# Kernel tuning notes

Hardware: AMD Instinct MI355X
Metric: run time of the kernel (lower is better)

## Reference

```python
import jax, jax.numpy as jnp
import numpy as np

HEADS = 30
HEAD_DIM = 64
DIM = HEADS * HEAD_DIM  # 1920
TXT = 226
VID = 2048
EPS = 1e-5


def setup_inputs() -> dict:
    key = jax.random.key(0)
    ks = jax.random.split(key, 12)
    s = 1.0 / np.sqrt(DIM)
    return {
        "hidden_states": jax.random.normal(ks[0], (1, VID, DIM), jnp.float32),
        "encoder_hidden_states": jax.random.normal(ks[1], (1, TXT, DIM), jnp.float32),
        "rope_cos": jax.random.uniform(ks[2], (VID, HEAD_DIM), jnp.float32, -1.0, 1.0),
        "rope_sin": jax.random.uniform(ks[3], (VID, HEAD_DIM), jnp.float32, -1.0, 1.0),
        "Wq": jax.random.normal(ks[4], (DIM, DIM), jnp.float32) * s,
        "bq": jnp.zeros((DIM,), jnp.float32),
        "Wk": jax.random.normal(ks[5], (DIM, DIM), jnp.float32) * s,
        "bk": jnp.zeros((DIM,), jnp.float32),
        "Wv": jax.random.normal(ks[6], (DIM, DIM), jnp.float32) * s,
        "bv": jnp.zeros((DIM,), jnp.float32),
        "ln_q_w": jnp.ones((HEAD_DIM,), jnp.float32),
        "ln_q_b": jnp.zeros((HEAD_DIM,), jnp.float32),
        "ln_k_w": jnp.ones((HEAD_DIM,), jnp.float32),
        "ln_k_b": jnp.zeros((HEAD_DIM,), jnp.float32),
        "Wo": jax.random.normal(ks[7], (DIM, DIM), jnp.float32) * s,
        "bo": jnp.zeros((DIM,), jnp.float32),
    }


def _layernorm(x, w, b):
    mu = jnp.mean(x, axis=-1, keepdims=True)
    var = jnp.var(x, axis=-1, keepdims=True)
    return (x - mu) * jax.lax.rsqrt(var + EPS) * w + b


def _apply_rope(x, cos, sin):
    # x: [B,H,S_vid,D]; cos/sin: [S_vid,D]. Interleaved-pair rotation (diffusers use_real, unbind_dim=-1).
    xr = x[..., 0::2]
    xi = x[..., 1::2]
    rot = jnp.stack([-xi, xr], axis=-1).reshape(x.shape)
    return x * cos + rot * sin


def reference(hidden_states, encoder_hidden_states, rope_cos, rope_sin,
              Wq, bq, Wk, bk, Wv, bv, ln_q_w, ln_q_b, ln_k_w, ln_k_b, Wo, bo):
    T = encoder_hidden_states.shape[1]
    h = jnp.concatenate([encoder_hidden_states, hidden_states], axis=1)  # [B,S,D]
    B, S, _ = h.shape

    def proj(W, bias):
        y = h @ W.T + bias
        return y.reshape(B, S, HEADS, HEAD_DIM).transpose(0, 2, 1, 3)  # [B,H,S,d]

    q = proj(Wq, bq)
    k = proj(Wk, bk)
    v = proj(Wv, bv)

    q = _layernorm(q, ln_q_w, ln_q_b)
    k = _layernorm(k, ln_k_w, ln_k_b)

    # rotary embedding applied only to the image/video tokens
    q = jnp.concatenate([q[:, :, :T], _apply_rope(q[:, :, T:], rope_cos, rope_sin)], axis=2)
    k = jnp.concatenate([k[:, :, :T], _apply_rope(k[:, :, T:], rope_cos, rope_sin)], axis=2)

    scale = 1.0 / np.sqrt(HEAD_DIM)
    scores = jnp.einsum("bhqd,bhkd->bhqk", q, k) * scale
    attn = jax.nn.softmax(scores, axis=-1)
    out = jnp.einsum("bhqk,bhkd->bhqd", attn, v)

    out = out.transpose(0, 2, 1, 3).reshape(B, S, DIM)
    out = out @ Wo.T + bo
    return out[:, T:], out[:, :T]
```

## Files before the change

### kernel.cpp

```cpp
#include <hip/hip_runtime.h>
#include <hip/hip_bf16.h>

typedef __hip_bfloat16 bf16;
using f32x4 = __attribute__((ext_vector_type(4))) float;
using f32x16 = __attribute__((ext_vector_type(16))) float;
using s16x8 = __attribute__((ext_vector_type(8))) short;

#define S_TOT 2274
#define S_PAD 2304
#define TTXT 226
#define DIMN 1920
#define NH 30
#define HD 64
#define NQKV 5760
#define QSCALE 0.1803368801f
#define NSPLIT 4
#define SMAX 20.0f

#define GLOAD_LDS16(g, l)                                                              \
  __builtin_amdgcn_global_load_lds((const __attribute__((address_space(1))) void*)(g), \
                                   (__attribute__((address_space(3))) void*)(l), 16, 0, 0)

__device__ __forceinline__ int xcd_swz(int orig, int nwg) {
  const int q = nwg >> 3, r = nwg & 7;
  const int xcd = orig & 7, pos = orig >> 3;
  return (xcd < r ? xcd * (q + 1) : r * (q + 1) + (xcd - r) * q) + pos;
}

__global__ void k_prep_all(const float* __restrict__ hid, const float* __restrict__ enc,
                           const float* __restrict__ Wq, const float* __restrict__ Wk,
                           const float* __restrict__ Wv, const float* __restrict__ Wo,
                           bf16* __restrict__ h_bf, bf16* __restrict__ wqkv,
                           bf16* __restrict__ wo_bf) {
  const long T1 = (long)S_PAD * DIMN;
  const long PER = (long)DIMN * DIMN;
  long i4 = ((long)blockIdx.x * blockDim.x + threadIdx.x) * 4;
  if (i4 >= T1 + 4 * PER) return;
  float4 v = make_float4(0.f, 0.f, 0.f, 0.f);
  bf16* dst;
  long di;
  if (i4 < T1) {
    int s = (int)(i4 / DIMN);
    if (s < TTXT)
      v = *reinterpret_cast<const float4*>(enc + i4);
    else if (s < S_TOT)
      v = *reinterpret_cast<const float4*>(hid + i4 - (long)TTXT * DIMN);
    dst = h_bf;
    di = i4;
  } else if (i4 < T1 + 3 * PER) {
    const long j = i4 - T1;
    const float* src = (j < PER) ? (Wq + j) : (j < 2 * PER) ? (Wk + j - PER) : (Wv + j - 2 * PER);
    v = *reinterpret_cast<const float4*>(src);
    dst = wqkv;
    di = j;
  } else {
    const long j = i4 - T1 - 3 * PER;
    v = *reinterpret_cast<const float4*>(Wo + j);
    dst = wo_bf;
    di = j;
  }
  union {
    bf16 b[4];
    short4 s4;
  } o;
  o.b[0] = __float2bfloat16(v.x);
  o.b[1] = __float2bfloat16(v.y);
  o.b[2] = __float2bfloat16(v.z);
  o.b[3] = __float2bfloat16(v.w);
  *reinterpret_cast<short4*>(dst + di) = o.s4;
}

#define NKT32 60
#define QBUF 24576
__global__ __launch_bounds__(512, 4) void k_gemm_qkv11(
    const bf16* __restrict__ A, const bf16* __restrict__ B, const float* __restrict__ bq,
    const float* __restrict__ bk, const float* __restrict__ bv, const float* __restrict__ lqw,
    const float* __restrict__ lqb, const float* __restrict__ lkw, const float* __restrict__ lkb,
    const float* __restrict__ cosT, const float* __restrict__ sinT, bf16* __restrict__ qb,
    bf16* __restrict__ kbf, bf16* __restrict__ vt) {
  __shared__ __align__(16) char smem[3 * QBUF];
  const int tid = threadIdx.x;
  const int w = tid >> 6, lane = tid & 63;
  const int clo = lane & 15, lhi = lane >> 4;
  const int wr = w >> 1, wc = w & 1;
  const int swz = xcd_swz(blockIdx.y * 45 + blockIdx.x, 405);
  const int m0 = (swz / 45) * 256, n0 = (swz % 45) * 128;

  const int u1 = 512 + tid;
  const long ga0 = (long)(m0 + (tid >> 2)) * DIMN + (((tid & 3) ^ ((tid >> 3) & 3)) * 8);
  const long ga1 = (long)(m0 + (u1 >> 2)) * DIMN + (((u1 & 3) ^ ((u1 >> 3) & 3)) * 8);
  const long gb0 = (long)(n0 + (tid >> 2)) * DIMN + (((tid & 3) ^ ((tid >> 3) & 3)) * 8);
  const int wbase = w * 1024;

  auto stage = [&](int b, int kt) {
    char* Ab = &smem[b * QBUF];
    char* Bb = Ab + 16384;
    const int ko = kt * 32;
    GLOAD_LDS16(A + ga0 + ko, Ab + wbase);
    GLOAD_LDS16(A + ga1 + ko, Ab + 8192 + wbase);
    GLOAD_LDS16(B + gb0 + ko, Bb + wbase);
  };

  auto rdf = [&](const char* base, int row) {
    return *reinterpret_cast<const s16x8*>(base + row * 64 + ((lhi ^ ((row >> 1) & 3)) * 16));
  };

  f32x4 acc[4][4] = {};

  stage(0, 0);
  stage(1, 1);
  for (int t = 0; t < NKT32; ++t) {
    if (t < NKT32 - 1)
      asm volatile("s_waitcnt vmcnt(3)" ::: "memory");
    else
      asm volatile("s_waitcnt vmcnt(0)" ::: "memory");
    __builtin_amdgcn_s_barrier();
    if (t + 2 < NKT32) stage((t + 2) % 3, t + 2);
    const char* Ab = &smem[(t % 3) * QBUF];
    const char* Bb = Ab + 16384;
    s16x8 af[4], bfr[4];
#pragma unroll
    for (int m = 0; m < 4; ++m) af[m] = rdf(Ab, wr * 64 + m * 16 + clo);
#pragma unroll
    for (int n = 0; n < 4; ++n) bfr[n] = rdf(Bb, wc * 64 + n * 16 + clo);
    __builtin_amdgcn_s_setprio(1);
#pragma unroll
    for (int m = 0; m < 4; ++m)
#pragma unroll
      for (int n = 0; n < 4; ++n)
        acc[m][n] = __builtin_amdgcn_mfma_f32_16x16x32_bf16(af[m], bfr[n], acc[m][n], 0, 0, 0);
    __builtin_amdgcn_s_setprio(0);
  }
  __syncthreads();

  const int gcol0 = n0 + wc * 64;
  const int sect = gcol0 / DIMN;
  const int hcol = gcol0 - sect * DIMN;
  const int head = hcol >> 6;
  const int row0 = m0 + wr * 64;

  if (sect < 2) {
    const float* bias = sect ? bk : bq;
    const float* lw = sect ? lkw : lqw;
    const float* lb = sect ? lkb : lqb;
    bf16* dst = sect ? kbf : qb;
    const float oscale = sect ? 1.f : QSCALE;
    float bb[4], lww[4], lbb[4];
#pragma unroll
    for (int n = 0; n < 4; ++n) {
      const int d = (n << 4) + clo;
      bb[n] = bias[hcol + d];
      lww[n] = lw[d];
      lbb[n] = lb[d];
    }
#pragma unroll
    for (int m = 0; m < 4; ++m) {
#pragma unroll
      for (int r = 0; r < 4; ++r) {
        const int row = row0 + m * 16 + lhi * 4 + r;
        float x[4];
#pragma unroll
        for (int n = 0; n < 4; ++n) x[n] = acc[m][n][r] + bb[n];
        float s_ = (x[0] + x[1]) + (x[2] + x[3]);
        float q_ = x[0] * x[0];
        q_ = fmaf(x[1], x[1], q_);
        q_ = fmaf(x[2], x[2], q_);
        q_ = fmaf(x[3], x[3], q_);
#pragma unroll
        for (int off = 1; off <= 8; off <<= 1) {
          s_ += __shfl_xor(s_, off);
          q_ += __shfl_xor(q_, off);
        }
        const float mu = s_ * (1.f / 64.f);
        const float var = q_ * (1.f / 64.f) - mu * mu;
        const float rst = rsqrtf(var + 1e-5f);
        float xn[4];
#pragma unroll
        for (int n = 0; n < 4; ++n) xn[n] = (x[n] - mu) * rst * lww[n] + lbb[n];
        const bool dorope = (row >= TTXT) && (row < S_TOT);
        if (dorope) {
          const float* cr = cosT + (long)(row - TTXT) * HD;
          const float* sr2 = sinT + (long)(row - TTXT) * HD;
#pragma unroll
          for (int n = 0; n < 4; ++n) {
            const int d = (n << 4) + clo;
            const float p = __shfl_xor(xn[n], 1);
            xn[n] = xn[n] * cr[d] + ((clo & 1) ? p : -p) * sr2[d];
          }
        }
#pragma unroll
        for (int n = 0; n < 4; ++n)
          dst[((long)head * S_PAD + row) * HD + (n << 4) + clo] =
              __float2bfloat16(xn[n] * oscale);
      }
    }
  } else {
    float bb[4];
#pragma unroll
    for (int n = 0; n < 4; ++n) bb[n] = bv[hcol + (n << 4) + clo];
    bf16* Lp = reinterpret_cast<bf16*>(smem + w * 9216);
#pragma unroll
    for (int m = 0; m < 4; ++m)
#pragma unroll
      for (int n = 0; n < 4; ++n)
#pragma unroll
        for (int r = 0; r < 4; ++r)
          Lp[((n << 4) + clo) * 72 + m * 16 + lhi * 4 + r] =
              __float2bfloat16(acc[m][n][r] + bb[n]);
    const int dsub = lane >> 3, sc = lane & 7;
#pragma unroll
    for (int it = 0; it < 8; ++it) {
      const int d = it * 8 + dsub;
      s16x8 v = *reinterpret_cast<const s16x8*>(&Lp[d * 72 + sc * 8]);
      *reinterpret_cast<s16x8*>(vt + ((long)head * HD + d) * S_PAD + row0 + sc * 8) = v;
    }
  }
}

__global__ __launch_bounds__(256, 4) void k_gemm_proj11(const bf16* __restrict__ A,
                                                        const bf16* __restrict__ B,
                                                        float* __restrict__ C,
                                                        const float* __restrict__ bias) {
  __shared__ __align__(16) char smem[3 * 12288];
  const int tid = threadIdx.x;
  const int w = tid >> 6, lane = tid & 63;
  const int clo = lane & 15, lhi = lane >> 4;
  const int wr = w >> 1, wc = w & 1;
  const int swz = xcd_swz(blockIdx.y * 30 + blockIdx.x, 540);
  const int m0 = (swz / 30) * 128, n0 = (swz % 30) * 64;

  const int u1 = 256 + tid;
  const long ga0 = (long)(m0 + (tid >> 2)) * DIMN + (((tid & 3) ^ ((tid >> 3) & 3)) * 8);
  const long ga1 = (long)(m0 + (u1 >> 2)) * DIMN + (((u1 & 3) ^ ((u1 >> 3) & 3)) * 8);
  const long gb0 = (long)(n0 + (tid >> 2)) * DIMN + (((tid & 3) ^ ((tid >> 3) & 3)) * 8);
  const int wbase = w * 1024;

  auto stage = [&](int b, int kt) {
    char* Ab = &smem[b * 12288];
    char* Bb = Ab + 8192;
    const int ko = kt * 32;
    GLOAD_LDS16(A + ga0 + ko, Ab + wbase);
    GLOAD_LDS16(A + ga1 + ko, Ab + 4096 + wbase);
    GLOAD_LDS16(B + gb0 + ko, Bb + wbase);
  };

  auto rdf = [&](const char* base, int row) {
    return *reinterpret_cast<const s16x8*>(base + row * 64 + ((lhi ^ ((row >> 1) & 3)) * 16));
  };

  f32x4 acc[4][2] = {};

  stage(0, 0);
  stage(1, 1);
  for (int t = 0; t < NKT32; ++t) {
    if (t < NKT32 - 1)
      asm volatile("s_waitcnt vmcnt(3)" ::: "memory");
    else
      asm volatile("s_waitcnt vmcnt(0)" ::: "memory");
    __builtin_amdgcn_s_barrier();
    if (t + 2 < NKT32) stage((t + 2) % 3, t + 2);
    const char* Ab = &smem[(t % 3) * 12288];
    const char* Bb = Ab + 8192;
    s16x8 af[4], bfr[2];
#pragma unroll
    for (int m = 0; m < 4; ++m) af[m] = rdf(Ab, wr * 64 + m * 16 + clo);
#pragma unroll
    for (int n = 0; n < 2; ++n) bfr[n] = rdf(Bb, wc * 32 + n * 16 + clo);
    __builtin_amdgcn_s_setprio(1);
#pragma unroll
    for (int m = 0; m < 4; ++m)
#pragma unroll
      for (int n = 0; n < 2; ++n)
        acc[m][n] = __builtin_amdgcn_mfma_f32_16x16x32_bf16(af[m], bfr[n], acc[m][n], 0, 0, 0);
    __builtin_amdgcn_s_setprio(0);
  }
#pragma unroll
  for (int n = 0; n < 2; ++n) {
    const int col = n0 + wc * 32 + n * 16 + clo;
    const float bvv = bias[col];
#pragma unroll
    for (int m = 0; m < 4; ++m) {
#pragma unroll
      for (int r = 0; r < 4; ++r) {
        const int row = m0 + wr * 64 + m * 16 + lhi * 4 + r;
        if (row < S_TOT) {
          const int dst = (row >= TTXT) ? (row - TTXT) : (row + (S_TOT - TTXT));
          C[(long)dst * DIMN + col] = acc[m][n][r] + bvv;
        }
      }
    }
  }
}

__global__ __launch_bounds__(512, 4) void k_flash14(const bf16* __restrict__ qb,
                                                    const bf16* __restrict__ kbf,
                                                    const bf16* __restrict__ vt,
                                                    bf16* __restrict__ po,
                                                    float* __restrict__ pl) {
  __shared__ __align__(16) char smem[32768];
  const int h = blockIdx.x, qt = blockIdx.y, ks = blockIdx.z;
  const int tid = threadIdx.x, w = tid >> 6, lane = tid & 63;
  const int l31 = lane & 31, hf = lane >> 5;
  const bf16* Qh = qb + (long)h * S_PAD * HD;
  const bf16* Kh = kbf + (long)h * S_PAD * HD;
  const bf16* Vh = vt + (long)h * HD * S_PAD;
  const int q0w = qt * 256 + w * 32;
  const int T0 = ks * 9;

  s16x8 qf[4];
#pragma unroll
  for (int t = 0; t < 4; ++t)
    qf[t] = *reinterpret_cast<const s16x8*>(Qh + (long)(q0w + l31) * HD + t * 16 + hf * 8);

  f32x16 accO[2] = {};
  f32x16 lacc = {};

  const s16x8 ones8 = {0x3F80, 0x3F80, 0x3F80, 0x3F80, 0x3F80, 0x3F80, 0x3F80, 0x3F80};

  const int sr = tid >> 3, sc8 = tid & 7;
  const long kg0 = (long)sr * HD + ((sc8 ^ (sr & 7)) * 8);
  const long vg0 = (long)sr * S_PAD + ((sc8 ^ (sr & 7)) * 8);
  const int ldsb = w * 1024;

  auto stage = [&](int b, int kb0) {
    char* Kb = &smem[b * 16384];
    char* Vb = &smem[b * 16384 + 8192];
    GLOAD_LDS16(Kh + (long)kb0 * HD + kg0, Kb + ldsb);
    GLOAD_LDS16(Vh + kb0 + vg0, Vb + ldsb);
  };

  auto ldsrd = [&](const char* base, int row, int c) {
    return *reinterpret_cast<const s16x8*>(base + row * 128 + ((c ^ (row & 7)) * 16));
  };
  auto pk2 = [&](float a, float b) -> unsigned {
    __hip_bfloat162 t = __float22bfloat162_rn(make_float2(a, b));
    return *reinterpret_cast<unsigned*>(&t);
  };

  stage(0, T0 * 64);
  __syncthreads();
  int cur = 0;
  for (int kt = 0; kt < 9; ++kt) {
    const int kb0 = (T0 + kt) * 64;
    if (kt + 1 < 9) stage(cur ^ 1, kb0 + 64);
    const char* Kb = &smem[cur * 16384];
    const char* Vb = &smem[cur * 16384 + 8192];

    f32x16 s0 = {}, s1 = {};
#pragma unroll
    for (int t = 0; t < 4; ++t) {
      s16x8 k0 = ldsrd(Kb, l31, 2 * t + hf);
      s16x8 k1 = ldsrd(Kb, 32 + l31, 2 * t + hf);
      s0 = __builtin_amdgcn_mfma_f32_32x32x16_bf16(k0, qf[t], s0, 0, 0, 0);
      s1 = __builtin_amdgcn_mfma_f32_32x32x16_bf16(k1, qf[t], s1, 0, 0, 0);
    }
    if (kb0 + 64 > S_TOT) {
#pragma unroll
      for (int j = 0; j < 16; ++j) {
        const int key = kb0 + (j & 3) + 8 * (j >> 2) + 4 * hf;
        if (key >= S_TOT) s0[j] = -1e30f;
        if (key + 32 >= S_TOT) s1[j] = -1e30f;
      }
    }
#pragma unroll
    for (int j = 0; j < 16; ++j) {
      s0[j] = exp2f(s0[j] - SMAX);
      s1[j] = exp2f(s1[j] - SMAX);
    }
    unsigned gw0[8], gw1[8];
#pragma unroll
    for (int i = 0; i < 4; ++i) {
      gw0[2 * i] = pk2(s0[4 * i], s0[4 * i + 1]);
      gw0[2 * i + 1] = pk2(s0[4 * i + 2], s0[4 * i + 3]);
      gw1[2 * i] = pk2(s1[4 * i], s1[4 * i + 1]);
      gw1[2 * i + 1] = pk2(s1[4 * i + 2], s1[4 * i + 3]);
    }
    s16x8 pa[4];
#pragma unroll
    for (int b = 0; b < 2; ++b) {
      unsigned* gw = b ? gw1 : gw0;
#pragma unroll
      for (int t = 0; t < 2; ++t) {
        auto rA = __builtin_amdgcn_permlane32_swap(gw[4 * t + 0], gw[4 * t + 2], false, false);
        auto rB = __builtin_amdgcn_permlane32_swap(gw[4 * t + 1], gw[4 * t + 3], false, false);
        union {
          unsigned u[4];
          s16x8 v;
        } A;
        A.u[0] = rA[0];
        A.u[1] = rB[0];
        A.u[2] = rA[1];
        A.u[3] = rB[1];
        pa[b * 2 + t] = A.v;
      }
    }
#pragma unroll
    for (int t4 = 0; t4 < 4; ++t4) {
      s16x8 v0 = ldsrd(Vb, l31, 2 * t4 + hf);
      s16x8 v1 = ldsrd(Vb, 32 + l31, 2 * t4 + hf);
      accO[0] = __builtin_amdgcn_mfma_f32_32x32x16_bf16(pa[t4], v0, accO[0], 0, 0, 0);
      accO[1] = __builtin_amdgcn_mfma_f32_32x32x16_bf16(pa[t4], v1, accO[1], 0, 0, 0);
      lacc = __builtin_amdgcn_mfma_f32_32x32x16_bf16(pa[t4], ones8, lacc, 0, 0, 0);
    }
    __syncthreads();
    cur ^= 1;
  }
  const long rowbase = ((long)(ks * NH + h)) * S_PAD + q0w;
  if (l31 == 0) {
#pragma unroll
    for (int j = 0; j < 16; ++j) pl[rowbase + (j & 3) + 8 * (j >> 2) + 4 * hf] = lacc[j];
  }
#pragma unroll
  for (int j = 0; j < 16; ++j) {
    const int pat = (j & 3) + 8 * (j >> 2) + 4 * hf;
    bf16* dst = po + (rowbase + pat) * HD + l31;
    dst[0] = __float2bfloat16(accO[0][j]);
    dst[32] = __float2bfloat16(accO[1][j]);
  }
}

__global__ __launch_bounds__(256) void k_combine4(const bf16* __restrict__ po,
                                                  const float* __restrict__ pl,
                                                  bf16* __restrict__ ao) {
  const int idx = blockIdx.x * 256 + threadIdx.x;
  const int d4 = (idx & 15) * 4;
  const int row = (idx >> 4) % S_PAD;
  const int h = idx / (S_PAD * 16);
  if (row >= S_TOT) return;
  float o[4] = {0.f, 0.f, 0.f, 0.f};
  float l = 0.f;
#pragma unroll
  for (int i = 0; i < NSPLIT; ++i) {
    const long r = ((long)(i * NH + h)) * S_PAD + row;
    const ushort4 p = *reinterpret_cast<const ushort4*>(po + r * HD + d4);
    o[0] += __uint_as_float((unsigned)p.x << 16);
    o[1] += __uint_as_float((unsigned)p.y << 16);
    o[2] += __uint_as_float((unsigned)p.z << 16);
    o[3] += __uint_as_float((unsigned)p.w << 16);
    l += pl[r];
  }
  const float inv = 1.f / l;
  union {
    bf16 b[4];
    short4 s4;
  } ob;
#pragma unroll
  for (int i = 0; i < 4; ++i) ob.b[i] = __float2bfloat16(o[i] * inv);
  *reinterpret_cast<short4*>(ao + (long)row * DIMN + h * HD + d4) = ob.s4;
}

extern "C" void kernel_launch(void* const* d_in, const int* in_sizes, int n_in, void* d_out,
                              int out_size, void* d_ws, size_t ws_size, hipStream_t stream) {
  const float* hid = (const float*)d_in[0];
  const float* enc = (const float*)d_in[1];
  const float* rc = (const float*)d_in[2];
  const float* rs = (const float*)d_in[3];
  const float* Wq = (const float*)d_in[4];
  const float* bq = (const float*)d_in[5];
  const float* Wk = (const float*)d_in[6];
  const float* bk = (const float*)d_in[7];
  const float* Wv = (const float*)d_in[8];
  const float* bv = (const float*)d_in[9];
  const float* lqw = (const float*)d_in[10];
  const float* lqb = (const float*)d_in[11];
  const float* lkw = (const float*)d_in[12];
  const float* lkb = (const float*)d_in[13];
  const float* Wo = (const float*)d_in[14];
  const float* bo = (const float*)d_in[15];
  float* out = (float*)d_out;

  char* ws = (char*)d_ws;
  size_t off = 0;
  bf16* po = (bf16*)(ws + off);
  off += (size_t)S_PAD * NQKV * 4;
  bf16* h_bf = (bf16*)(ws + off);
  off += (size_t)S_PAD * DIMN * 2;
  bf16* wqkv = (bf16*)(ws + off);
  off += (size_t)3 * DIMN * DIMN * 2;
  bf16* wo = (bf16*)(ws + off);
  off += (size_t)DIMN * DIMN * 2;
  bf16* q_bf = (bf16*)(ws + off);
  off += (size_t)NH * S_PAD * HD * 2;
  bf16* k_bf = (bf16*)(ws + off);
  off += (size_t)NH * S_PAD * HD * 2;
  bf16* vt_bf = (bf16*)(ws + off);
  off += (size_t)NH * HD * S_PAD * 2;
  bf16* at_bf = (bf16*)(ws + off);
  off += (size_t)S_PAD * DIMN * 2;

  float* pl = (float*)h_bf;

  const long PREP_N = ((long)S_PAD * DIMN + 4L * DIMN * DIMN) / 4;
  k_prep_all<<<(int)((PREP_N + 255) / 256), 256, 0, stream>>>(hid, enc, Wq, Wk, Wv, Wo, h_bf,
                                                              wqkv, wo);
  k_gemm_qkv11<<<dim3(45, 9), 512, 0, stream>>>(h_bf, wqkv, bq, bk, bv, lqw, lqb, lkw, lkb, rc,
                                                rs, q_bf, k_bf, vt_bf);
  k_flash14<<<dim3(NH, S_PAD / 256, NSPLIT), 512, 0, stream>>>(q_bf, k_bf, vt_bf, po, pl);
  k_combine4<<<NH * S_PAD * 16 / 256, 256, 0, stream>>>(po, pl, at_bf);
  k_gemm_proj11<<<dim3(30, 18), 256, 0, stream>>>(at_bf, wo, out, bo);
}
```

Before: 213.3 us.

## Deepen QKV GEMM K-tile to 64 and interleave loads with MFMA quadrants

```diff
diff --git a/kernel.cpp b/kernel.cpp
--- a/kernel.cpp
+++ b/kernel.cpp
@@ -70,15 +70,16 @@
   *reinterpret_cast<short4*>(dst + di) = o.s4;
 }
 
-#define NKT32 60
-#define QBUF 24576
-__global__ __launch_bounds__(512, 4) void k_gemm_qkv11(
+#define NKT64 30
+#define ABYTES 32768
+#define TBUF 49152
+__global__ __launch_bounds__(512, 1) void k_gemm_qkv12(
     const bf16* __restrict__ A, const bf16* __restrict__ B, const float* __restrict__ bq,
     const float* __restrict__ bk, const float* __restrict__ bv, const float* __restrict__ lqw,
     const float* __restrict__ lqb, const float* __restrict__ lkw, const float* __restrict__ lkb,
     const float* __restrict__ cosT, const float* __restrict__ sinT, bf16* __restrict__ qb,
     bf16* __restrict__ kbf, bf16* __restrict__ vt) {
-  __shared__ __align__(16) char smem[3 * QBUF];
+  __shared__ __align__(16) char smem[3 * TBUF];
   const int tid = threadIdx.x;
   const int w = tid >> 6, lane = tid & 63;
   const int clo = lane & 15, lhi = lane >> 4;
@@ -86,50 +87,135 @@
   const int swz = xcd_swz(blockIdx.y * 45 + blockIdx.x, 405);
   const int m0 = (swz / 45) * 256, n0 = (swz % 45) * 128;
 
-  const int u1 = 512 + tid;
-  const long ga0 = (long)(m0 + (tid >> 2)) * DIMN + (((tid & 3) ^ ((tid >> 3) & 3)) * 8);
-  const long ga1 = (long)(m0 + (u1 >> 2)) * DIMN + (((u1 & 3) ^ ((u1 >> 3) & 3)) * 8);
-  const long gb0 = (long)(n0 + (tid >> 2)) * DIMN + (((tid & 3) ^ ((tid >> 3) & 3)) * 8);
+  long ga[4], gb[2];
+#pragma unroll
+  for (int i = 0; i < 4; ++i) {
+    const int u = i * 512 + tid;
+    ga[i] = (long)(m0 + (u >> 3)) * DIMN + (((u & 7) ^ ((u >> 3) & 7)) * 8);
+  }
+#pragma unroll
+  for (int i = 0; i < 2; ++i) {
+    const int u = i * 512 + tid;
+    gb[i] = (long)(n0 + (u >> 3)) * DIMN + (((u & 7) ^ ((u >> 3) & 7)) * 8);
+  }
   const int wbase = w * 1024;
 
-  auto stage = [&](int b, int kt) {
-    char* Ab = &smem[b * QBUF];
-    char* Bb = Ab + 16384;
-    const int ko = kt * 32;
-    GLOAD_LDS16(A + ga0 + ko, Ab + wbase);
-    GLOAD_LDS16(A + ga1 + ko, Ab + 8192 + wbase);
-    GLOAD_LDS16(B + gb0 + ko, Bb + wbase);
-  };
-
-  auto rdf = [&](const char* base, int row) {
-    return *reinterpret_cast<const s16x8*>(base + row * 64 + ((lhi ^ ((row >> 1) & 3)) * 16));
+  auto stA = [&](int b, int kt, int i) {
+    GLOAD_LDS16(A + ga[i] + kt * 64, &smem[b * TBUF] + i * 8192 + wbase);
+  };
+  auto stB = [&](int b, int kt, int i) {
+    GLOAD_LDS16(B + gb[i] + kt * 64, &smem[b * TBUF] + ABYTES + i * 8192 + wbase);
+  };
+  auto stageAll = [&](int b, int kt) {
+#pragma unroll
+    for (int i = 0; i < 4; ++i) stA(b, kt, i);
+#pragma unroll
+    for (int i = 0; i < 2; ++i) stB(b, kt, i);
+  };
+
+  auto rdA = [&](const char* buf, int m, int k) {
+    const int row = wr * 64 + m * 16 + clo;
+    return *reinterpret_cast<const s16x8*>(buf + row * 128 + (((k * 4 + lhi) ^ (row & 7)) * 16));
+  };
+  auto rdB = [&](const char* buf, int n, int k) {
+    const int row = wc * 64 + n * 16 + clo;
+    return *reinterpret_cast<const s16x8*>(buf + ABYTES + row * 128 +
+                                           (((k * 4 + lhi) ^ (row & 7)) * 16));
   };
 
   f32x4 acc[4][4] = {};
-
-  stage(0, 0);
-  stage(1, 1);
-  for (int t = 0; t < NKT32; ++t) {
-    if (t < NKT32 - 1)
-      asm volatile("s_waitcnt vmcnt(3)" ::: "memory");
+  s16x8 a01[2][2], a23[2][2], b01[2][2], b23[2][2];
+
+  stageAll(0, 0);
+  stageAll(1, 1);
+  asm volatile("s_waitcnt vmcnt(6)" ::: "memory");
+  __builtin_amdgcn_s_barrier();
+
+  for (int t = 0; t < NKT64; ++t) {
+    const char* buf = &smem[(t % 3) * TBUF];
+    const bool pre = (t + 2 < NKT64);
+    const int nb = (t + 2) % 3;
+#pragma unroll
+    for (int m = 0; m < 2; ++m)
+#pragma unroll
+      for (int k = 0; k < 2; ++k) a01[m][k] = rdA(buf, m, k);
+#pragma unroll
+    for (int n = 0; n < 2; ++n)
+#pragma unroll
+      for (int k = 0; k < 2; ++k) b01[n][k] = rdB(buf, n, k);
+    if (pre) {
+      stA(nb, t + 2, 0);
+      stA(nb, t + 2, 1);
+    }
+    __builtin_amdgcn_s_barrier();
+    asm volatile("s_waitcnt lgkmcnt(0)" ::: "memory");
+    __builtin_amdgcn_s_setprio(1);
+#pragma unroll
+    for (int m = 0; m < 2; ++m)
+#pragma unroll
+      for (int n = 0; n < 2; ++n)
+#pragma unroll
+        for (int k = 0; k < 2; ++k)
+          acc[m][n] = __builtin_amdgcn_mfma_f32_16x16x32_bf16(a01[m][k], b01[n][k], acc[m][n], 0, 0, 0);
+    __builtin_amdgcn_s_setprio(0);
+    __builtin_amdgcn_s_barrier();
+#pragma unroll
+    for (int n = 0; n < 2; ++n)
+#pragma unroll
+      for (int k = 0; k < 2; ++k) b23[n][k] = rdB(buf, n + 2, k);
+    if (pre) {
+      stA(nb, t + 2, 2);
+      stA(nb, t + 2, 3);
+    }
+    __builtin_amdgcn_s_barrier();
+    asm volatile("s_waitcnt lgkmcnt(0)" ::: "memory");
+    __builtin_amdgcn_s_setprio(1);
+#pragma unroll
+    for (int m = 0; m < 2; ++m)
+#pragma unroll
+      for (int n = 0; n < 2; ++n)
+#pragma unroll
+        for (int k = 0; k < 2; ++k)
+          acc[m][n + 2] =
+              __builtin_amdgcn_mfma_f32_16x16x32_bf16(a01[m][k], b23[n][k], acc[m][n + 2], 0, 0, 0);
+    __builtin_amdgcn_s_setprio(0);
+    __builtin_amdgcn_s_barrier();
+#pragma unroll
+    for (int m = 0; m < 2; ++m)
+#pragma unroll
+      for (int k = 0; k < 2; ++k) a23[m][k] = rdA(buf, m + 2, k);
+    if (pre) {
+      stB(nb, t + 2, 0);
+      stB(nb, t + 2, 1);
+    }
+    __builtin_amdgcn_s_barrier();
+    asm volatile("s_waitcnt lgkmcnt(0)" ::: "memory");
+    __builtin_amdgcn_s_setprio(1);
+#pragma unroll
+    for (int m = 0; m < 2; ++m)
+#pragma unroll
+      for (int n = 0; n < 2; ++n)
+#pragma unroll
+        for (int k = 0; k < 2; ++k)
+          acc[m + 2][n] =
+              __builtin_amdgcn_mfma_f32_16x16x32_bf16(a23[m][k], b01[n][k], acc[m + 2][n], 0, 0, 0);
+    __builtin_amdgcn_s_setprio(0);
+    __builtin_amdgcn_s_barrier();
+    __builtin_amdgcn_s_setprio(1);
+#pragma unroll
+    for (int m = 0; m < 2; ++m)
+#pragma unroll
+      for (int n = 0; n < 2; ++n)
+#pragma unroll
+        for (int k = 0; k < 2; ++k)
+          acc[m + 2][n + 2] = __builtin_amdgcn_mfma_f32_16x16x32_bf16(a23[m][k], b23[n][k],
+                                                                     acc[m + 2][n + 2], 0, 0, 0);
+    __builtin_amdgcn_s_setprio(0);
+    if (pre)
+      asm volatile("s_waitcnt vmcnt(6)" ::: "memory");
     else
       asm volatile("s_waitcnt vmcnt(0)" ::: "memory");
     __builtin_amdgcn_s_barrier();
-    if (t + 2 < NKT32) stage((t + 2) % 3, t + 2);
-    const char* Ab = &smem[(t % 3) * QBUF];
-    const char* Bb = Ab + 16384;
-    s16x8 af[4], bfr[4];
-#pragma unroll
-    for (int m = 0; m < 4; ++m) af[m] = rdf(Ab, wr * 64 + m * 16 + clo);
-#pragma unroll
-    for (int n = 0; n < 4; ++n) bfr[n] = rdf(Bb, wc * 64 + n * 16 + clo);
-    __builtin_amdgcn_s_setprio(1);
-#pragma unroll
-    for (int m = 0; m < 4; ++m)
-#pragma unroll
-      for (int n = 0; n < 4; ++n)
-        acc[m][n] = __builtin_amdgcn_mfma_f32_16x16x32_bf16(af[m], bfr[n], acc[m][n], 0, 0, 0);
-    __builtin_amdgcn_s_setprio(0);
   }
   __syncthreads();
 
@@ -217,6 +303,7 @@
   }
 }
 
+#define NKT32 60
 __global__ __launch_bounds__(256, 4) void k_gemm_proj11(const bf16* __restrict__ A,
                                                         const bf16* __restrict__ B,
                                                         float* __restrict__ C,
@@ -493,7 +580,7 @@
   const long PREP_N = ((long)S_PAD * DIMN + 4L * DIMN * DIMN) / 4;
   k_prep_all<<<(int)((PREP_N + 255) / 256), 256, 0, stream>>>(hid, enc, Wq, Wk, Wv, Wo, h_bf,
                                                               wqkv, wo);
-  k_gemm_qkv11<<<dim3(45, 9), 512, 0, stream>>>(h_bf, wqkv, bq, bk, bv, lqw, lqb, lkw, lkb, rc,
+  k_gemm_qkv12<<<dim3(45, 9), 512, 0, stream>>>(h_bf, wqkv, bq, bk, bv, lqw, lqb, lkw, lkb, rc,
                                                 rs, q_bf, k_bf, vt_bf);
   k_flash14<<<dim3(NH, S_PAD / 256, NSPLIT), 512, 0, stream>>>(q_bf, k_bf, vt_bf, po, pl);
   k_combine4<<<NH * S_PAD * 16 / 256, 256, 0, stream>>>(po, pl, at_bf);
```

Measured after the change: 220.9 us. 1.04x slower.
